# Kernel optimization log

Measured on AMD Instinct MI355X. Metric: run time of the kernel, lower is better.

The kernel has to match this reference:

```python
import jax, jax.numpy as jnp
from jax import lax
import numpy as np

V, S, B, E, H = 32000, 256, 16, 32, 16
KEEP = 0.6  # 1 - dropout_percent (0.4)


def setup_inputs() -> dict:
    key = jax.random.key(0)
    ks = jax.random.split(key, 11)
    stdv = 1.0 / np.sqrt(H)  # init_params: uniform(-stdv, stdv) for ALL params
    u = lambda k, shp: jax.random.uniform(k, shp, jnp.float32, -stdv, stdv)
    return {
        "input_batch": jax.random.randint(ks[0], (S, B), 0, V),
        "mask_lr": jax.random.bernoulli(ks[1], KEEP, (S, B, H)).astype(jnp.float32),
        "mask_rl": jax.random.bernoulli(ks[2], KEEP, (S, B, H)).astype(jnp.float32),
        "embedding": u(ks[3], (V, E)),
        "W_ih_lr": u(ks[4], (E + H, H)),
        "b_ih_lr": u(ks[5], (H,)),
        "W_ih_rl": u(ks[6], (E + H, H)),
        "b_ih_rl": u(ks[7], (H,)),
        "W_ho": u(ks[8], (2 * H, V)),
        "b_ho": u(ks[9], (V,)),
        "initial_hidden": u(ks[10], (1, H)),
    }


def _make_step(W, b):
    def step(h, xm):
        w, m = xm  # w: [B,E] embedded token, m: [B,H] dropout keep-mask
        h_new = jnp.tanh(jnp.concatenate([w, h], axis=1) @ W + b)
        h_new = h_new * (m / KEEP)  # inverted dropout, matches mul by mask then 1/(1-p)
        return h_new, h_new
    return step


def reference(input_batch, mask_lr, mask_rl, embedding, W_ih_lr, b_ih_lr,
              W_ih_rl, b_ih_rl, W_ho, b_ho, initial_hidden):
    emb = embedding[input_batch]                       # [S,B,E]
    h0 = jnp.broadcast_to(lax.stop_gradient(initial_hidden), (B, H))  # .data.expand in torch

    # left-to-right: s_lr[t] = hLR[t+1] (state after consuming token t)
    _, s_lr = lax.scan(_make_step(W_ih_lr, b_ih_lr), h0, (emb, mask_lr))
    # right-to-left over reversed sequence, then flip: s_rl[t] = hRL[t]
    _, s_rl_rev = lax.scan(_make_step(W_ih_rl, b_ih_rl), h0,
                           (emb[::-1], mask_rl[::-1]))
    s_rl = jnp.flip(s_rl_rev, 0)

    # prediction at i uses hLR[i] and hRL[i+1]
    hLR_used = jnp.concatenate([h0[None], s_lr[:-1]], axis=0)  # [S,B,H]
    hRL_used = jnp.concatenate([s_rl[1:], h0[None]], axis=0)   # [S,B,H]
    hcat = jnp.concatenate([hLR_used, hRL_used], axis=-1)      # [S,B,2H]

    logits = jnp.einsum('sbh,hv->sbv', hcat, W_ho) + b_ho      # [S,B,V]
    return jax.nn.log_softmax(logits, axis=-1)
```

## Files before the change

### kernel.cpp

```cpp
#include <hip/hip_runtime.h>
#include <hip/hip_bf16.h>
#include <math.h>

#define V 32000
#define S 256
#define B 16
#define E 32
#define H 16
#define INV_KEEP (1.0f / 0.6f)
#define MR (S * B)
#define NVT (V / 16)

typedef __bf16 bf16x8 __attribute__((ext_vector_type(8)));
typedef float  f32x4  __attribute__((ext_vector_type(4)));

static __device__ __forceinline__ float ldf(const float* p, int i) { return p[i]; }
static __device__ __forceinline__ float ldf(const __hip_bfloat16* p, int i) { return __bfloat162float(p[i]); }
static __device__ __forceinline__ void stf(float* p, size_t i, float v) { p[i] = v; }
static __device__ __forceinline__ void stf(__hip_bfloat16* p, size_t i, float v) { p[i] = __float2bfloat16(v); }

__global__ void detect_kernel(const unsigned int* __restrict__ emb_words,
                              int* __restrict__ flag) {
    int lane = threadIdx.x;
    unsigned int w = emb_words[lane];
    unsigned int lo = w & 0xFFFFu;
    unsigned int ab = lo & 0x7FFFu;
    int hit = (ab == 0u) || (ab >= 0x3000u && ab <= 0x3E80u);
    unsigned long long m = __ballot(hit != 0);
    if (lane == 0) flag[0] = (__popcll(m) >= 32) ? 1 : 0;
}

template <typename T>
__global__ void precompute_kernel(const int* __restrict__ tok,
                                  const T* __restrict__ emb,
                                  const T* __restrict__ W_lr,
                                  const T* __restrict__ b_lr,
                                  const T* __restrict__ W_rl,
                                  const T* __restrict__ b_rl,
                                  float* __restrict__ pre,
                                  const int* __restrict__ flag, int want) {
    if (flag[0] != want) return;
    int id = blockIdx.x * blockDim.x + threadIdx.x;
    if (id >= 2 * S * B * H) return;
    int dir = id >> 16;
    int rem = id & 0xFFFF;
    int t = rem >> 8;
    int b = (rem >> 4) & 15;
    int i = rem & 15;
    const T* Wp = dir ? W_rl : W_lr;
    const T* bp = dir ? b_rl : b_lr;
    int tk = tok[t * B + b];
    const T* er = emb + (size_t)tk * E;
    float acc = ldf(bp, i);
#pragma unroll
    for (int e = 0; e < E; ++e)
        acc += ldf(er, e) * ldf(Wp, e * H + i);
    pre[id] = acc;
}

template <int J>
static __device__ __forceinline__ float grp_bcast(float h) {
#if __has_builtin(__builtin_amdgcn_ds_swizzle)
    return __uint_as_float(__builtin_amdgcn_ds_swizzle(
        __float_as_uint(h), (J << 5) | 0x10));
#else
    int lane = threadIdx.x & 63;
    return __shfl(h, (lane & ~15) | J, 64);
#endif
}
static __device__ __forceinline__ float fast_rcp(float x) {
#if __has_builtin(__builtin_amdgcn_rcpf)
    return __builtin_amdgcn_rcpf(x);
#else
    return 1.f / x;
#endif
}
static __device__ __forceinline__ float fast_tanh(float x) {
    x = fminf(fmaxf(x, -15.f), 15.f);
    float e = __expf(2.f * x);
    return 1.f - 2.f * fast_rcp(e + 1.f);
}

template <typename T>
__global__ void scan_kernel(const float* __restrict__ pre,
                            const T* __restrict__ mask_lr,
                            const T* __restrict__ mask_rl,
                            const T* __restrict__ W_lr,
                            const T* __restrict__ W_rl,
                            const T* __restrict__ h0,
                            float* __restrict__ sarr,
                            const int* __restrict__ flag, int want) {
    if (flag[0] != want) return;
    int dir = blockIdx.x;
    int tid = threadIdx.x;
    int b = tid >> 4;
    int i = tid & 15;
    const T* Wp = dir ? W_rl : W_lr;
    const T* mk = dir ? mask_rl : mask_lr;
    float wh[H];
#pragma unroll
    for (int j = 0; j < H; ++j) wh[j] = ldf(Wp, (E + j) * H + i);
    float h = ldf(h0, i);
    const float* pred = pre + dir * (S * B * H);
    float* sd = sarr + dir * (S * B * H);

    int base = b * 16 + i;
    int step = dir ? -256 : 256;
    int idx = (dir ? (S - 1) * 256 : 0) + base;

    float pA = pred[idx];
    float mA = ldf(mk, idx) * INV_KEEP;
    float pB = pred[idx + step];
    float mB = ldf(mk, idx + step) * INV_KEEP;

    for (int k = 0; k < S; ++k) {
        float pN = 0.f, mN = 0.f;
        if (k + 2 < S) {
            int idn = idx + 2 * step;
            pN = pred[idn];
            mN = ldf(mk, idn) * INV_KEEP;
        }
        float s0 = grp_bcast<0>(h) * wh[0];
        s0 += grp_bcast<1>(h) * wh[1];
        s0 += grp_bcast<2>(h) * wh[2];
        s0 += grp_bcast<3>(h) * wh[3];
        float s1 = grp_bcast<4>(h) * wh[4];
        s1 += grp_bcast<5>(h) * wh[5];
        s1 += grp_bcast<6>(h) * wh[6];
        s1 += grp_bcast<7>(h) * wh[7];
        float s2 = grp_bcast<8>(h) * wh[8];
        s2 += grp_bcast<9>(h) * wh[9];
        s2 += grp_bcast<10>(h) * wh[10];
        s2 += grp_bcast<11>(h) * wh[11];
        float s3 = grp_bcast<12>(h) * wh[12];
        s3 += grp_bcast<13>(h) * wh[13];
        s3 += grp_bcast<14>(h) * wh[14];
        s3 += grp_bcast<15>(h) * wh[15];
        float acc = pA + ((s0 + s1) + (s2 + s3));
        h = fast_tanh(acc) * mA;
        sd[idx] = h;
        pA = pB; mA = mB; pB = pN; mB = mN;
        idx += step;
    }
}

template <typename T>
__global__ void pack_kernel(const float* __restrict__ sarr,
                            const T* __restrict__ h0,
                            __bf16* __restrict__ hi,
                            __bf16* __restrict__ lo,
                            const int* __restrict__ flag, int want) {
    if (flag[0] != want) return;
    int id = blockIdx.x * blockDim.x + threadIdx.x;
    int k = id & 31;
    int row = id >> 5;
    int t = row >> 4, b = row & 15;
    const float* s0 = sarr;
    const float* s1 = sarr + S * B * H;
    float v;
    if (k < H)
        v = (t == 0) ? ldf(h0, k) : s0[(t - 1) * 256 + b * 16 + k];
    else
        v = (t == S - 1) ? ldf(h0, k - H) : s1[(t + 1) * 256 + b * 16 + (k - H)];
    __bf16 h = (__bf16)v;
    hi[id] = h;
    lo[id] = (__bf16)(v - (float)h);
}

__global__ void zero_kernel(float* __restrict__ se) {
    int i = blockIdx.x * 256 + threadIdx.x;
    if (i < MR) se[i] = 0.f;
}

template <typename T>
__global__ void wpack_kernel(const T* __restrict__ W_ho,
                             const T* __restrict__ b_ho,
                             __bf16* __restrict__ wph,
                             __bf16* __restrict__ wpl,
                             float* __restrict__ bsf,
                             const int* __restrict__ flag, int want) {
    if (flag[0] != want) return;
    int id = blockIdx.x * blockDim.x + threadIdx.x;
    if (id < NVT * 64) {
        int c = id & 15, g = (id >> 4) & 3, vt = id >> 6;
        int v = vt * 16 + c;
        bf16x8 h8, l8;
#pragma unroll
        for (int j = 0; j < 8; ++j) {
            float w = ldf(W_ho, (size_t)(g * 8 + j) * V + v);
            __bf16 wh = (__bf16)w;
            h8[j] = wh;
            l8[j] = (__bf16)(w - (float)wh);
        }
        *(bf16x8*)(wph + (size_t)id * 8) = h8;
        *(bf16x8*)(wpl + (size_t)id * 8) = l8;
    } else {
        int v = id - NVT * 64;
        if (v < V) bsf[v] = ldf(b_ho, v);
    }
}

__global__ __launch_bounds__(256) void lse_packed_kernel(
        const __bf16* __restrict__ hi, const __bf16* __restrict__ lo,
        const __bf16* __restrict__ wph, const __bf16* __restrict__ wpl,
        const float* __restrict__ bsf,
        float* __restrict__ se) {
    int sbt = blockIdx.x >> 3;
    int vch = blockIdx.x & 7;
    int wave = threadIdx.x >> 6;
    int l = threadIdx.x & 63;
    int c = l & 15, g = l >> 4;
    int aoff = (sbt * 16 + c) * 32 + g * 8;
    bf16x8 ah = *(const bf16x8*)(hi + aoff);
    bf16x8 al = *(const bf16x8*)(lo + aoff);
    float part[4] = {0.f, 0.f, 0.f, 0.f};
    int vt_end = (vch + 1) * (NVT / 8);
    for (int vt = vch * (NVT / 8) + wave; vt < vt_end; vt += 4) {
        int woff = ((vt * 4 + g) * 16 + c) * 8;
        bf16x8 bh = *(const bf16x8*)(wph + woff);
        bf16x8 bl = *(const bf16x8*)(wpl + woff);
        f32x4 acc = {0.f, 0.f, 0.f, 0.f};
        acc = __builtin_amdgcn_mfma_f32_16x16x32_bf16(ah, bh, acc, 0, 0, 0);
        acc = __builtin_amdgcn_mfma_f32_16x16x32_bf16(al, bh, acc, 0, 0, 0);
        acc = __builtin_amdgcn_mfma_f32_16x16x32_bf16(ah, bl, acc, 0, 0, 0);
        float bb = bsf[vt * 16 + c];
#pragma unroll
        for (int r = 0; r < 4; ++r) part[r] += __expf(acc[r] + bb);
    }
#pragma unroll
    for (int r = 0; r < 4; ++r) {
        float p = part[r];
        p += __shfl_xor(p, 1, 64);
        p += __shfl_xor(p, 2, 64);
        p += __shfl_xor(p, 4, 64);
        p += __shfl_xor(p, 8, 64);
        if (c == 0) atomicAdd(&se[sbt * 16 + g * 4 + r], p);
    }
}

__global__ void log_kernel(float* __restrict__ se) {
    int i = blockIdx.x * 256 + threadIdx.x;
    if (i < MR) se[i] = logf(se[i]);
}

template <typename T>
__global__ __launch_bounds__(64) void write_packed_kernel(
        const __bf16* __restrict__ hi, const __bf16* __restrict__ lo,
        const __bf16* __restrict__ wph, const __bf16* __restrict__ wpl,
        const float* __restrict__ bsf,
        const float* __restrict__ lse, T* __restrict__ out,
        const int* __restrict__ flag, int want) {
    if (flag[0] != want) return;
    int vt = blockIdx.x >> 2;
    int sc = blockIdx.x & 3;
    int l = threadIdx.x;
    int c = l & 15, g = l >> 4;
    int v0 = vt * 16;
    int woff = ((vt * 4 + g) * 16 + c) * 8;
    bf16x8 bh = *(const bf16x8*)(wph + woff);
    bf16x8 bl = *(const bf16x8*)(wpl + woff);
    float bb = bsf[v0 + c];
    int sb_end = sc * 64 + 64;
    for (int sbt = sc * 64; sbt < sb_end; ++sbt) {
        int aoff = (sbt * 16 + c) * 32 + g * 8;
        bf16x8 ah = *(const bf16x8*)(hi + aoff);
        bf16x8 al = *(const bf16x8*)(lo + aoff);
        f32x4 acc = {0.f, 0.f, 0.f, 0.f};
        acc = __builtin_amdgcn_mfma_f32_16x16x32_bf16(ah, bh, acc, 0, 0, 0);
        acc = __builtin_amdgcn_mfma_f32_16x16x32_bf16(al, bh, acc, 0, 0, 0);
        acc = __builtin_amdgcn_mfma_f32_16x16x32_bf16(ah, bl, acc, 0, 0, 0);
#pragma unroll
        for (int r = 0; r < 4; ++r) {
            int row = sbt * 16 + g * 4 + r;
            stf(out, (size_t)row * V + v0 + c, acc[r] + bb - lse[row]);
        }
    }
}

template <typename T>
__global__ __launch_bounds__(256) void lse_kernel(
        const __bf16* __restrict__ hi, const __bf16* __restrict__ lo,
        const T* __restrict__ W_ho, const T* __restrict__ b_ho,
        float* __restrict__ se,
        const int* __restrict__ flag, int want) {
    if (flag[0] != want) return;
    int sbt = blockIdx.x >> 3;
    int vch = blockIdx.x & 7;
    int wave = threadIdx.x >> 6;
    int l = threadIdx.x & 63;
    int c = l & 15, g = l >> 4;
    int aoff = (sbt * 16 + c) * 32 + g * 8;
    bf16x8 ah = *(const bf16x8*)(hi + aoff);
    bf16x8 al = *(const bf16x8*)(lo + aoff);
    float part[4] = {0.f, 0.f, 0.f, 0.f};
    int vt_end = (vch + 1) * (NVT / 8);
    for (int vt = vch * (NVT / 8) + wave; vt < vt_end; vt += 4) {
        int v0 = vt * 16;
        const T* wp = W_ho + (g * 8) * V + v0 + c;
        bf16x8 bh, bl;
#pragma unroll
        for (int j = 0; j < 8; ++j) {
            float w = ldf(wp, j * V);
            __bf16 wh = (__bf16)w;
            bh[j] = wh;
            bl[j] = (__bf16)(w - (float)wh);
        }
        f32x4 acc = {0.f, 0.f, 0.f, 0.f};
        acc = __builtin_amdgcn_mfma_f32_16x16x32_bf16(ah, bh, acc, 0, 0, 0);
        acc = __builtin_amdgcn_mfma_f32_16x16x32_bf16(al, bh, acc, 0, 0, 0);
        acc = __builtin_amdgcn_mfma_f32_16x16x32_bf16(ah, bl, acc, 0, 0, 0);
        float bb = ldf(b_ho, v0 + c);
#pragma unroll
        for (int r = 0; r < 4; ++r) part[r] += __expf(acc[r] + bb);
    }
#pragma unroll
    for (int r = 0; r < 4; ++r) {
        float p = part[r];
        p += __shfl_xor(p, 1, 64);
        p += __shfl_xor(p, 2, 64);
        p += __shfl_xor(p, 4, 64);
        p += __shfl_xor(p, 8, 64);
        if (c == 0) atomicAdd(&se[sbt * 16 + g * 4 + r], p);
    }
}

template <typename T>
__global__ __launch_bounds__(64) void write_kernel(
        const __bf16* __restrict__ hi, const __bf16* __restrict__ lo,
        const T* __restrict__ W_ho, const T* __restrict__ b_ho,
        const float* __restrict__ lse, T* __restrict__ out,
        const int* __restrict__ flag, int want) {
    if (flag[0] != want) return;
    int vt = blockIdx.x >> 2;
    int sc = blockIdx.x & 3;
    int l = threadIdx.x;
    int c = l & 15, g = l >> 4;
    int v0 = vt * 16;
    const T* wp = W_ho + (g * 8) * V + v0 + c;
    bf16x8 bh, bl;
#pragma unroll
    for (int j = 0; j < 8; ++j) {
        float w = ldf(wp, j * V);
        __bf16 wh = (__bf16)w;
        bh[j] = wh;
        bl[j] = (__bf16)(w - (float)wh);
    }
    float bb = ldf(b_ho, v0 + c);
    int sb_end = sc * 64 + 64;
    for (int sbt = sc * 64; sbt < sb_end; ++sbt) {
        int aoff = (sbt * 16 + c) * 32 + g * 8;
        bf16x8 ah = *(const bf16x8*)(hi + aoff);
        bf16x8 al = *(const bf16x8*)(lo + aoff);
        f32x4 acc = {0.f, 0.f, 0.f, 0.f};
        acc = __builtin_amdgcn_mfma_f32_16x16x32_bf16(ah, bh, acc, 0, 0, 0);
        acc = __builtin_amdgcn_mfma_f32_16x16x32_bf16(al, bh, acc, 0, 0, 0);
        acc = __builtin_amdgcn_mfma_f32_16x16x32_bf16(ah, bl, acc, 0, 0, 0);
#pragma unroll
        for (int r = 0; r < 4; ++r) {
            int row = sbt * 16 + g * 4 + r;
            stf(out, (size_t)row * V + v0 + c, acc[r] + bb - lse[row]);
        }
    }
}

extern "C" void kernel_launch(void* const* d_in, const int* in_sizes, int n_in,
                              void* d_out, int out_size, void* d_ws, size_t ws_size,
                              hipStream_t stream) {
    const int* tok = (const int*)d_in[0];

    char* wsb      = (char*)d_ws;
    float* pre     = (float*)wsb;
    float* sarr    = (float*)(wsb + (512u << 10));
    __bf16* hcb_hi = (__bf16*)wsb;
    __bf16* hcb_lo = (__bf16*)(wsb + (256u << 10));
    float* se      = sarr;
    int*   flag    = (int*)(wsb + (1u << 20));
    __bf16* wph    = (__bf16*)(wsb + (2u << 20));
    __bf16* wpl    = (__bf16*)(wsb + (4u << 20));
    float* bsf     = (float*)(wsb + (6u << 20));
    const bool packed = ws_size >= ((size_t)8u << 20);

    detect_kernel<<<1, 64, 0, stream>>>((const unsigned int*)d_in[3], flag);

    if (packed) {
        wpack_kernel<float><<<625, 256, 0, stream>>>(
            (const float*)d_in[8], (const float*)d_in[9], wph, wpl, bsf, flag, 0);
        wpack_kernel<__hip_bfloat16><<<625, 256, 0, stream>>>(
            (const __hip_bfloat16*)d_in[8], (const __hip_bfloat16*)d_in[9], wph, wpl, bsf, flag, 1);
    }

    {
        const float* mask_lr = (const float*)d_in[1];
        const float* mask_rl = (const float*)d_in[2];
        const float* emb     = (const float*)d_in[3];
        const float* W_lr    = (const float*)d_in[4];
        const float* b_lr    = (const float*)d_in[5];
        const float* W_rl    = (const float*)d_in[6];
        const float* b_rl    = (const float*)d_in[7];
        const float* h0      = (const float*)d_in[10];
        precompute_kernel<float><<<512, 256, 0, stream>>>(tok, emb, W_lr, b_lr, W_rl, b_rl, pre, flag, 0);
        scan_kernel<float><<<2, 256, 0, stream>>>(pre, mask_lr, mask_rl, W_lr, W_rl, h0, sarr, flag, 0);
        pack_kernel<float><<<512, 256, 0, stream>>>(sarr, h0, hcb_hi, hcb_lo, flag, 0);
    }

    {
        const __hip_bfloat16* mask_lr = (const __hip_bfloat16*)d_in[1];
        const __hip_bfloat16* mask_rl = (const __hip_bfloat16*)d_in[2];
        const __hip_bfloat16* emb     = (const __hip_bfloat16*)d_in[3];
        const __hip_bfloat16* W_lr    = (const __hip_bfloat16*)d_in[4];
        const __hip_bfloat16* b_lr    = (const __hip_bfloat16*)d_in[5];
        const __hip_bfloat16* W_rl    = (const __hip_bfloat16*)d_in[6];
        const __hip_bfloat16* b_rl    = (const __hip_bfloat16*)d_in[7];
        const __hip_bfloat16* h0      = (const __hip_bfloat16*)d_in[10];
        precompute_kernel<__hip_bfloat16><<<512, 256, 0, stream>>>(tok, emb, W_lr, b_lr, W_rl, b_rl, pre, flag, 1);
        scan_kernel<__hip_bfloat16><<<2, 256, 0, stream>>>(pre, mask_lr, mask_rl, W_lr, W_rl, h0, sarr, flag, 1);
        pack_kernel<__hip_bfloat16><<<512, 256, 0, stream>>>(sarr, h0, hcb_hi, hcb_lo, flag, 1);
    }

    zero_kernel<<<16, 256, 0, stream>>>(se);

    if (packed) {
        lse_packed_kernel<<<2048, 256, 0, stream>>>(hcb_hi, hcb_lo, wph, wpl, bsf, se);
        log_kernel<<<16, 256, 0, stream>>>(se);
        write_packed_kernel<float><<<8000, 64, 0, stream>>>(
            hcb_hi, hcb_lo, wph, wpl, bsf, se, (float*)d_out, flag, 0);
        write_packed_kernel<__hip_bfloat16><<<8000, 64, 0, stream>>>(
            hcb_hi, hcb_lo, wph, wpl, bsf, se, (__hip_bfloat16*)d_out, flag, 1);
    } else {
        lse_kernel<float><<<2048, 256, 0, stream>>>(
            hcb_hi, hcb_lo, (const float*)d_in[8], (const float*)d_in[9], se, flag, 0);
        lse_kernel<__hip_bfloat16><<<2048, 256, 0, stream>>>(
            hcb_hi, hcb_lo, (const __hip_bfloat16*)d_in[8], (const __hip_bfloat16*)d_in[9], se, flag, 1);
        log_kernel<<<16, 256, 0, stream>>>(se);
        write_kernel<float><<<8000, 64, 0, stream>>>(
            hcb_hi, hcb_lo, (const float*)d_in[8], (const float*)d_in[9], se, (float*)d_out, flag, 0);
        write_kernel<__hip_bfloat16><<<8000, 64, 0, stream>>>(
            hcb_hi, hcb_lo, (const __hip_bfloat16*)d_in[8], (const __hip_bfloat16*)d_in[9], se, (__hip_bfloat16*)d_out, flag, 1);
    }
}
```

Measured before the change: 848.4 us.

## Merge dtype-specialized kernels into runtime-dispatched launches and widen write tiles

Replaces each pair of float/bf16 kernel launches with a single kernel that branches on the device-side dtype flag, cutting the launch count. The zero-fill of the row-sum buffer is folded into the weight-pack kernel, and that buffer moves to its own workspace slot so it no longer aliases the scan output. The output-writing kernel now processes four vocab tiles per block (2000 blocks instead of 8000), reusing each loaded activation fragment across four MFMA groups. In exchange it uses more registers per thread and launches fewer blocks.

```diff
diff --git a/kernel.cpp b/kernel.cpp
--- a/kernel.cpp
+++ b/kernel.cpp
@@ -31,15 +31,11 @@
 }
 
 template <typename T>
-__global__ void precompute_kernel(const int* __restrict__ tok,
-                                  const T* __restrict__ emb,
-                                  const T* __restrict__ W_lr,
-                                  const T* __restrict__ b_lr,
-                                  const T* __restrict__ W_rl,
-                                  const T* __restrict__ b_rl,
-                                  float* __restrict__ pre,
-                                  const int* __restrict__ flag, int want) {
-    if (flag[0] != want) return;
+static __device__ __forceinline__ void precompute_body(
+        const int* __restrict__ tok, const T* __restrict__ emb,
+        const T* __restrict__ W_lr, const T* __restrict__ b_lr,
+        const T* __restrict__ W_rl, const T* __restrict__ b_rl,
+        float* __restrict__ pre) {
     int id = blockIdx.x * blockDim.x + threadIdx.x;
     if (id >= 2 * S * B * H) return;
     int dir = id >> 16;
@@ -58,6 +54,22 @@
     pre[id] = acc;
 }
 
+__global__ void precompute_u_kernel(const int* __restrict__ tok,
+                                    const void* emb,
+                                    const void* W_lr, const void* b_lr,
+                                    const void* W_rl, const void* b_rl,
+                                    float* __restrict__ pre,
+                                    const int* __restrict__ flag) {
+    if (flag[0])
+        precompute_body<__hip_bfloat16>(tok, (const __hip_bfloat16*)emb,
+            (const __hip_bfloat16*)W_lr, (const __hip_bfloat16*)b_lr,
+            (const __hip_bfloat16*)W_rl, (const __hip_bfloat16*)b_rl, pre);
+    else
+        precompute_body<float>(tok, (const float*)emb,
+            (const float*)W_lr, (const float*)b_lr,
+            (const float*)W_rl, (const float*)b_rl, pre);
+}
+
 template <int J>
 static __device__ __forceinline__ float grp_bcast(float h) {
 #if __has_builtin(__builtin_amdgcn_ds_swizzle)
@@ -82,15 +94,11 @@
 }
 
 template <typename T>
-__global__ void scan_kernel(const float* __restrict__ pre,
-                            const T* __restrict__ mask_lr,
-                            const T* __restrict__ mask_rl,
-                            const T* __restrict__ W_lr,
-                            const T* __restrict__ W_rl,
-                            const T* __restrict__ h0,
-                            float* __restrict__ sarr,
-                            const int* __restrict__ flag, int want) {
-    if (flag[0] != want) return;
+static __device__ __forceinline__ void scan_body(
+        const float* __restrict__ pre,
+        const T* __restrict__ mask_lr, const T* __restrict__ mask_rl,
+        const T* __restrict__ W_lr, const T* __restrict__ W_rl,
+        const T* __restrict__ h0, float* __restrict__ sarr) {
     int dir = blockIdx.x;
     int tid = threadIdx.x;
     int b = tid >> 4;
@@ -144,13 +152,24 @@
     }
 }
 
-template <typename T>
-__global__ void pack_kernel(const float* __restrict__ sarr,
-                            const T* __restrict__ h0,
-                            __bf16* __restrict__ hi,
-                            __bf16* __restrict__ lo,
-                            const int* __restrict__ flag, int want) {
-    if (flag[0] != want) return;
+__global__ void scan_u_kernel(const float* __restrict__ pre,
+                              const void* mask_lr, const void* mask_rl,
+                              const void* W_lr, const void* W_rl,
+                              const void* h0, float* __restrict__ sarr,
+                              const int* __restrict__ flag) {
+    if (flag[0])
+        scan_body<__hip_bfloat16>(pre, (const __hip_bfloat16*)mask_lr,
+            (const __hip_bfloat16*)mask_rl, (const __hip_bfloat16*)W_lr,
+            (const __hip_bfloat16*)W_rl, (const __hip_bfloat16*)h0, sarr);
+    else
+        scan_body<float>(pre, (const float*)mask_lr, (const float*)mask_rl,
+            (const float*)W_lr, (const float*)W_rl, (const float*)h0, sarr);
+}
+
+template <typename T>
+static __device__ __forceinline__ void pack_body(
+        const float* __restrict__ sarr, const T* __restrict__ h0,
+        __bf16* __restrict__ hi, __bf16* __restrict__ lo) {
     int id = blockIdx.x * blockDim.x + threadIdx.x;
     int k = id & 31;
     int row = id >> 5;
@@ -167,19 +186,23 @@
     lo[id] = (__bf16)(v - (float)h);
 }
 
+__global__ void pack_u_kernel(const float* __restrict__ sarr, const void* h0,
+                              __bf16* __restrict__ hi, __bf16* __restrict__ lo,
+                              const int* __restrict__ flag) {
+    if (flag[0]) pack_body<__hip_bfloat16>(sarr, (const __hip_bfloat16*)h0, hi, lo);
+    else         pack_body<float>(sarr, (const float*)h0, hi, lo);
+}
+
 __global__ void zero_kernel(float* __restrict__ se) {
     int i = blockIdx.x * 256 + threadIdx.x;
     if (i < MR) se[i] = 0.f;
 }
 
 template <typename T>
-__global__ void wpack_kernel(const T* __restrict__ W_ho,
-                             const T* __restrict__ b_ho,
-                             __bf16* __restrict__ wph,
-                             __bf16* __restrict__ wpl,
-                             float* __restrict__ bsf,
-                             const int* __restrict__ flag, int want) {
-    if (flag[0] != want) return;
+static __device__ __forceinline__ void wpack_body(
+        const T* __restrict__ W_ho, const T* __restrict__ b_ho,
+        __bf16* __restrict__ wph, __bf16* __restrict__ wpl,
+        float* __restrict__ bsf) {
     int id = blockIdx.x * blockDim.x + threadIdx.x;
     if (id < NVT * 64) {
         int c = id & 15, g = (id >> 4) & 3, vt = id >> 6;
@@ -198,6 +221,19 @@
         int v = id - NVT * 64;
         if (v < V) bsf[v] = ldf(b_ho, v);
     }
+}
+
+__global__ void wpack_u_kernel(const void* W_ho, const void* b_ho,
+                               __bf16* __restrict__ wph, __bf16* __restrict__ wpl,
+                               float* __restrict__ bsf, float* __restrict__ se,
+                               const int* __restrict__ flag) {
+    int id = blockIdx.x * blockDim.x + threadIdx.x;
+    if (id < MR) se[id] = 0.f;
+    if (flag[0])
+        wpack_body<__hip_bfloat16>((const __hip_bfloat16*)W_ho,
+                                   (const __hip_bfloat16*)b_ho, wph, wpl, bsf);
+    else
+        wpack_body<float>((const float*)W_ho, (const float*)b_ho, wph, wpl, bsf);
 }
 
 __global__ __launch_bounds__(256) void lse_packed_kernel(
@@ -243,38 +279,73 @@
     if (i < MR) se[i] = logf(se[i]);
 }
 
-template <typename T>
-__global__ __launch_bounds__(64) void write_packed_kernel(
+template <typename OT>
+static __device__ __forceinline__ void write_body(
         const __bf16* __restrict__ hi, const __bf16* __restrict__ lo,
         const __bf16* __restrict__ wph, const __bf16* __restrict__ wpl,
-        const float* __restrict__ bsf,
-        const float* __restrict__ lse, T* __restrict__ out,
-        const int* __restrict__ flag, int want) {
-    if (flag[0] != want) return;
-    int vt = blockIdx.x >> 2;
+        const float* __restrict__ bsf, const float* __restrict__ lse,
+        OT* __restrict__ out) {
+    int vq = blockIdx.x >> 2;
     int sc = blockIdx.x & 3;
     int l = threadIdx.x;
     int c = l & 15, g = l >> 4;
-    int v0 = vt * 16;
-    int woff = ((vt * 4 + g) * 16 + c) * 8;
-    bf16x8 bh = *(const bf16x8*)(wph + woff);
-    bf16x8 bl = *(const bf16x8*)(wpl + woff);
-    float bb = bsf[v0 + c];
+    int vt0 = vq * 4;
+    bf16x8 bh0, bl0, bh1, bl1, bh2, bl2, bh3, bl3;
+    float bb0, bb1, bb2, bb3;
+    {
+        int w0 = (((vt0 + 0) * 4 + g) * 16 + c) * 8;
+        int w1 = (((vt0 + 1) * 4 + g) * 16 + c) * 8;
+        int w2 = (((vt0 + 2) * 4 + g) * 16 + c) * 8;
+        int w3 = (((vt0 + 3) * 4 + g) * 16 + c) * 8;
+        bh0 = *(const bf16x8*)(wph + w0); bl0 = *(const bf16x8*)(wpl + w0);
+        bh1 = *(const bf16x8*)(wph + w1); bl1 = *(const bf16x8*)(wpl + w1);
+        bh2 = *(const bf16x8*)(wph + w2); bl2 = *(const bf16x8*)(wpl + w2);
+        bh3 = *(const bf16x8*)(wph + w3); bl3 = *(const bf16x8*)(wpl + w3);
+        bb0 = bsf[(vt0 + 0) * 16 + c];
+        bb1 = bsf[(vt0 + 1) * 16 + c];
+        bb2 = bsf[(vt0 + 2) * 16 + c];
+        bb3 = bsf[(vt0 + 3) * 16 + c];
+    }
     int sb_end = sc * 64 + 64;
     for (int sbt = sc * 64; sbt < sb_end; ++sbt) {
         int aoff = (sbt * 16 + c) * 32 + g * 8;
         bf16x8 ah = *(const bf16x8*)(hi + aoff);
         bf16x8 al = *(const bf16x8*)(lo + aoff);
-        f32x4 acc = {0.f, 0.f, 0.f, 0.f};
-        acc = __builtin_amdgcn_mfma_f32_16x16x32_bf16(ah, bh, acc, 0, 0, 0);
-        acc = __builtin_amdgcn_mfma_f32_16x16x32_bf16(al, bh, acc, 0, 0, 0);
-        acc = __builtin_amdgcn_mfma_f32_16x16x32_bf16(ah, bl, acc, 0, 0, 0);
+        f32x4 a0 = {0.f, 0.f, 0.f, 0.f}, a1 = a0, a2 = a0, a3 = a0;
+        a0 = __builtin_amdgcn_mfma_f32_16x16x32_bf16(ah, bh0, a0, 0, 0, 0);
+        a1 = __builtin_amdgcn_mfma_f32_16x16x32_bf16(ah, bh1, a1, 0, 0, 0);
+        a2 = __builtin_amdgcn_mfma_f32_16x16x32_bf16(ah, bh2, a2, 0, 0, 0);
+        a3 = __builtin_amdgcn_mfma_f32_16x16x32_bf16(ah, bh3, a3, 0, 0, 0);
+        a0 = __builtin_amdgcn_mfma_f32_16x16x32_bf16(al, bh0, a0, 0, 0, 0);
+        a1 = __builtin_amdgcn_mfma_f32_16x16x32_bf16(al, bh1, a1, 0, 0, 0);
+        a2 = __builtin_amdgcn_mfma_f32_16x16x32_bf16(al, bh2, a2, 0, 0, 0);
+        a3 = __builtin_amdgcn_mfma_f32_16x16x32_bf16(al, bh3, a3, 0, 0, 0);
+        a0 = __builtin_amdgcn_mfma_f32_16x16x32_bf16(ah, bl0, a0, 0, 0, 0);
+        a1 = __builtin_amdgcn_mfma_f32_16x16x32_bf16(ah, bl1, a1, 0, 0, 0);
+        a2 = __builtin_amdgcn_mfma_f32_16x16x32_bf16(ah, bl2, a2, 0, 0, 0);
+        a3 = __builtin_amdgcn_mfma_f32_16x16x32_bf16(ah, bl3, a3, 0, 0, 0);
 #pragma unroll
         for (int r = 0; r < 4; ++r) {
             int row = sbt * 16 + g * 4 + r;
-            stf(out, (size_t)row * V + v0 + c, acc[r] + bb - lse[row]);
+            float ls = lse[row];
+            size_t base = (size_t)row * V + vt0 * 16 + c;
+            stf(out, base,      a0[r] + bb0 - ls);
+            stf(out, base + 16, a1[r] + bb1 - ls);
+            stf(out, base + 32, a2[r] + bb2 - ls);
+            stf(out, base + 48, a3[r] + bb3 - ls);
         }
     }
+}
+
+__global__ __launch_bounds__(64) void write_u_kernel(
+        const __bf16* __restrict__ hi, const __bf16* __restrict__ lo,
+        const __bf16* __restrict__ wph, const __bf16* __restrict__ wpl,
+        const float* __restrict__ bsf, const float* __restrict__ lse,
+        void* out, const int* __restrict__ flag) {
+    if (flag[0])
+        write_body<__hip_bfloat16>(hi, lo, wph, wpl, bsf, lse, (__hip_bfloat16*)out);
+    else
+        write_body<float>(hi, lo, wph, wpl, bsf, lse, (float*)out);
 }
 
 template <typename T>
@@ -373,60 +444,34 @@
     float* sarr    = (float*)(wsb + (512u << 10));
     __bf16* hcb_hi = (__bf16*)wsb;
     __bf16* hcb_lo = (__bf16*)(wsb + (256u << 10));
-    float* se      = sarr;
     int*   flag    = (int*)(wsb + (1u << 20));
     __bf16* wph    = (__bf16*)(wsb + (2u << 20));
     __bf16* wpl    = (__bf16*)(wsb + (4u << 20));
     float* bsf     = (float*)(wsb + (6u << 20));
+    float* sep     = (float*)(wsb + (7u << 20));
     const bool packed = ws_size >= ((size_t)8u << 20);
 
     detect_kernel<<<1, 64, 0, stream>>>((const unsigned int*)d_in[3], flag);
 
     if (packed) {
-        wpack_kernel<float><<<625, 256, 0, stream>>>(
-            (const float*)d_in[8], (const float*)d_in[9], wph, wpl, bsf, flag, 0);
-        wpack_kernel<__hip_bfloat16><<<625, 256, 0, stream>>>(
-            (const __hip_bfloat16*)d_in[8], (const __hip_bfloat16*)d_in[9], wph, wpl, bsf, flag, 1);
-    }
-
-    {
-        const float* mask_lr = (const float*)d_in[1];
-        const float* mask_rl = (const float*)d_in[2];
-        const float* emb     = (const float*)d_in[3];
-        const float* W_lr    = (const float*)d_in[4];
-        const float* b_lr    = (const float*)d_in[5];
-        const float* W_rl    = (const float*)d_in[6];
-        const float* b_rl    = (const float*)d_in[7];
-        const float* h0      = (const float*)d_in[10];
-        precompute_kernel<float><<<512, 256, 0, stream>>>(tok, emb, W_lr, b_lr, W_rl, b_rl, pre, flag, 0);
-        scan_kernel<float><<<2, 256, 0, stream>>>(pre, mask_lr, mask_rl, W_lr, W_rl, h0, sarr, flag, 0);
-        pack_kernel<float><<<512, 256, 0, stream>>>(sarr, h0, hcb_hi, hcb_lo, flag, 0);
-    }
-
-    {
-        const __hip_bfloat16* mask_lr = (const __hip_bfloat16*)d_in[1];
-        const __hip_bfloat16* mask_rl = (const __hip_bfloat16*)d_in[2];
-        const __hip_bfloat16* emb     = (const __hip_bfloat16*)d_in[3];
-        const __hip_bfloat16* W_lr    = (const __hip_bfloat16*)d_in[4];
-        const __hip_bfloat16* b_lr    = (const __hip_bfloat16*)d_in[5];
-        const __hip_bfloat16* W_rl    = (const __hip_bfloat16*)d_in[6];
-        const __hip_bfloat16* b_rl    = (const __hip_bfloat16*)d_in[7];
-        const __hip_bfloat16* h0      = (const __hip_bfloat16*)d_in[10];
-        precompute_kernel<__hip_bfloat16><<<512, 256, 0, stream>>>(tok, emb, W_lr, b_lr, W_rl, b_rl, pre, flag, 1);
-        scan_kernel<__hip_bfloat16><<<2, 256, 0, stream>>>(pre, mask_lr, mask_rl, W_lr, W_rl, h0, sarr, flag, 1);
-        pack_kernel<__hip_bfloat16><<<512, 256, 0, stream>>>(sarr, h0, hcb_hi, hcb_lo, flag, 1);
-    }
-
-    zero_kernel<<<16, 256, 0, stream>>>(se);
-
-    if (packed) {
-        lse_packed_kernel<<<2048, 256, 0, stream>>>(hcb_hi, hcb_lo, wph, wpl, bsf, se);
-        log_kernel<<<16, 256, 0, stream>>>(se);
-        write_packed_kernel<float><<<8000, 64, 0, stream>>>(
-            hcb_hi, hcb_lo, wph, wpl, bsf, se, (float*)d_out, flag, 0);
-        write_packed_kernel<__hip_bfloat16><<<8000, 64, 0, stream>>>(
-            hcb_hi, hcb_lo, wph, wpl, bsf, se, (__hip_bfloat16*)d_out, flag, 1);
+        wpack_u_kernel<<<625, 256, 0, stream>>>(d_in[8], d_in[9], wph, wpl, bsf, sep, flag);
+        precompute_u_kernel<<<512, 256, 0, stream>>>(tok, d_in[3], d_in[4], d_in[5],
+                                                     d_in[6], d_in[7], pre, flag);
+        scan_u_kernel<<<2, 256, 0, stream>>>(pre, d_in[1], d_in[2], d_in[4],
+                                             d_in[6], d_in[10], sarr, flag);
+        pack_u_kernel<<<512, 256, 0, stream>>>(sarr, d_in[10], hcb_hi, hcb_lo, flag);
+        lse_packed_kernel<<<2048, 256, 0, stream>>>(hcb_hi, hcb_lo, wph, wpl, bsf, sep);
+        log_kernel<<<16, 256, 0, stream>>>(sep);
+        write_u_kernel<<<2000, 64, 0, stream>>>(hcb_hi, hcb_lo, wph, wpl, bsf, sep,
+                                                d_out, flag);
     } else {
+        float* se = sarr;
+        precompute_u_kernel<<<512, 256, 0, stream>>>(tok, d_in[3], d_in[4], d_in[5],
+                                                     d_in[6], d_in[7], pre, flag);
+        scan_u_kernel<<<2, 256, 0, stream>>>(pre, d_in[1], d_in[2], d_in[4],
+                                             d_in[6], d_in[10], sarr, flag);
+        pack_u_kernel<<<512, 256, 0, stream>>>(sarr, d_in[10], hcb_hi, hcb_lo, flag);
+        zero_kernel<<<16, 256, 0, stream>>>(se);
         lse_kernel<float><<<2048, 256, 0, stream>>>(
             hcb_hi, hcb_lo, (const float*)d_in[8], (const float*)d_in[9], se, flag, 0);
         lse_kernel<__hip_bfloat16><<<2048, 256, 0, stream>>>(
```

New measurement: 733.4 us. 13.6% less time.
